# Kernel tuning notes

Measured on AMD Instinct MI355X. Metric: run time of the kernel, lower is better.

## Reference

```python
import jax, jax.numpy as jnp
import numpy as np

N = 1048576
B = 1024
H = 128
EPS = 1e-12  # F.normalize default eps


def setup_inputs() -> dict:
    key = jax.random.key(0)
    k1, k2, k3 = jax.random.split(key, 3)
    emb = jax.random.normal(k1, (N, H), dtype=jnp.float32)
    summary = jax.random.normal(k2, (B, H), dtype=jnp.float32)
    # CSR-style ptr: 0 = ptr[0] <= ... <= ptr[B] = N
    inner = jnp.sort(jax.random.randint(k3, (B - 1,), 0, N))
    ptr = jnp.concatenate([jnp.zeros((1,), jnp.int64),
                           inner.astype(jnp.int64),
                           jnp.full((1,), N, jnp.int64)])
    d = jnp.ones((H,), dtype=jnp.float32)
    scale = jnp.ones((1,), dtype=jnp.float32)
    return {"emb": emb, "summary": summary, "ptr": ptr, "d": d, "scale": scale}


def reference(emb, summary, ptr, d, scale):
    # L2-normalize each row (torch F.normalize: x / max(||x||, eps))
    norm = jnp.linalg.norm(emb, axis=-1, keepdims=True)
    emb_n = emb / jnp.maximum(norm, EPS)
    # node -> graph segment id from ptr (node i belongs to segment s iff ptr[s] <= i < ptr[s+1])
    seg = jnp.searchsorted(ptr[1:], jnp.arange(emb.shape[0]), side="right")  # [N]
    # fused diag-scale + per-graph ragged dot: out[n] = sum_h emb_n[n,h] * d[h] * summary[seg[n],h]
    s_per_node = summary[seg]  # [N, H] gather
    sim = jnp.sum(emb_n * d[None, :] * s_per_node, axis=-1)  # [N]
    return sim * scale[0]
```

## Files before the change

kernel.cpp:

```cpp
#include <hip/hip_runtime.h>
#include <math.h>


#define HDIM 128
#define NEPS 1e-12f
#define ROWS_PER_BLOCK 32

__global__ __launch_bounds__(256) void sim_fused(
    const float* __restrict__ emb,
    const float* __restrict__ summary,
    const int*   __restrict__ ptr,
    const float* __restrict__ dvec,
    const float* __restrict__ scale,
    float* __restrict__ out, int N, int B)
{
    __shared__ int s_bounds[2];

    const long long row0 = (long long)blockIdx.x * ROWS_PER_BLOCK;

    if (threadIdx.x < 2) {
        long long r = row0 + (threadIdx.x ? ROWS_PER_BLOCK - 1 : 0);
        if (r > (long long)N - 1) r = (long long)N - 1;
        int lo = 0, hi = B;
        while (lo < hi) {
            int mid = (lo + hi) >> 1;
            if (ptr[1 + mid] <= (int)r) lo = mid + 1; else hi = mid;
        }
        s_bounds[threadIdx.x] = lo;
    }
    __syncthreads();
    const int s0 = s_bounds[0];
    const int s1 = s_bounds[1];

    const int sub = threadIdx.x & 7;
    const long long row = row0 + (threadIdx.x >> 3);
    if (row >= N) return;

    int s = s0;
    while (s < s1 && ptr[s + 1] <= (int)row) ++s;

    const float4* e4 = (const float4*)(emb + row * (long long)HDIM);
    const float4* w4 = (const float4*)(summary + (long long)s * HDIM);
    const float4* d4 = (const float4*)dvec;

    float sumsq = 0.f, dot = 0.f;
    #pragma unroll
    for (int j = 0; j < 4; ++j) {
        const float4 e  = e4[sub + 8 * j];
        const float4 w  = w4[sub + 8 * j];
        const float4 dd = d4[sub + 8 * j];
        sumsq = fmaf(e.x, e.x, sumsq); sumsq = fmaf(e.y, e.y, sumsq);
        sumsq = fmaf(e.z, e.z, sumsq); sumsq = fmaf(e.w, e.w, sumsq);
        dot = fmaf(e.x, w.x * dd.x, dot); dot = fmaf(e.y, w.y * dd.y, dot);
        dot = fmaf(e.z, w.z * dd.z, dot); dot = fmaf(e.w, w.w * dd.w, dot);
    }
    #pragma unroll
    for (int m = 4; m >= 1; m >>= 1) {
        sumsq += __shfl_xor(sumsq, m, 64);
        dot   += __shfl_xor(dot,   m, 64);
    }
    if (sub == 0)
        out[row] = dot / fmaxf(sqrtf(sumsq), NEPS) * scale[0];
}

extern "C" void kernel_launch(void* const* d_in, const int* in_sizes, int n_in,
                              void* d_out, int out_size, void* d_ws, size_t ws_size,
                              hipStream_t stream) {
    const float* emb     = (const float*)d_in[0];
    const float* summary = (const float*)d_in[1];
    const int*   ptr     = (const int*)d_in[2];
    const float* dvec    = (const float*)d_in[3];
    const float* scale   = (const float*)d_in[4];
    float*       out     = (float*)d_out;

    const int Hn = in_sizes[3];
    const int N  = in_sizes[0] / Hn;
    const int B  = in_sizes[1] / Hn;

    (void)d_ws; (void)ws_size; (void)n_in; (void)out_size;

    sim_fused<<<(N + ROWS_PER_BLOCK - 1) / ROWS_PER_BLOCK, 256, 0, stream>>>(
        emb, summary, ptr, dvec, scale, out, N, B);
}
```

Measured before the change: 689.7 us.

## Use half-wave per row with batched nontemporal loads and single-segment fast path

Reorganizes work so each half-wave handles one row with one float4 per lane, and each thread issues eight independent row loads up front to raise memory-level parallelism. Rows per block double to 64. Streaming loads and stores are marked nontemporal to avoid polluting cache. A fast path skips the per-row segment search when the whole block lies in one segment, at the cost of more registers and longer shuffle reductions.

```diff
diff --git a/kernel.cpp b/kernel.cpp
--- a/kernel.cpp
+++ b/kernel.cpp
@@ -4,7 +4,9 @@
 
 #define HDIM 128
 #define NEPS 1e-12f
-#define ROWS_PER_BLOCK 32
+#define ROWS_PER_BLOCK 64
+
+typedef float f4v __attribute__((ext_vector_type(4)));
 
 __global__ __launch_bounds__(256) void sim_fused(
     const float* __restrict__ emb,
@@ -32,35 +34,71 @@
     const int s0 = s_bounds[0];
     const int s1 = s_bounds[1];
 
-    const int sub = threadIdx.x & 7;
-    const long long row = row0 + (threadIdx.x >> 3);
-    if (row >= N) return;
+    const int wave = threadIdx.x >> 6;
+    const int lane = threadIdx.x & 63;
+    const int half = lane >> 5;
+    const int l    = lane & 31;
+    const float sc = scale[0];
 
-    int s = s0;
-    while (s < s1 && ptr[s + 1] <= (int)row) ++s;
+    const long long rbase = row0 + 2 * wave + half;
 
-    const float4* e4 = (const float4*)(emb + row * (long long)HDIM);
-    const float4* w4 = (const float4*)(summary + (long long)s * HDIM);
-    const float4* d4 = (const float4*)dvec;
+    f4v e[8];
+    #pragma unroll
+    for (int it = 0; it < 8; ++it) {
+        const long long row = rbase + 8 * it;
+        const f4v* p = (const f4v*)(emb + row * (long long)HDIM) + l;
+        e[it] = (row < N) ? __builtin_nontemporal_load(p) : (f4v)(0.f);
+    }
 
-    float sumsq = 0.f, dot = 0.f;
-    #pragma unroll
-    for (int j = 0; j < 4; ++j) {
-        const float4 e  = e4[sub + 8 * j];
-        const float4 w  = w4[sub + 8 * j];
-        const float4 dd = d4[sub + 8 * j];
-        sumsq = fmaf(e.x, e.x, sumsq); sumsq = fmaf(e.y, e.y, sumsq);
-        sumsq = fmaf(e.z, e.z, sumsq); sumsq = fmaf(e.w, e.w, sumsq);
-        dot = fmaf(e.x, w.x * dd.x, dot); dot = fmaf(e.y, w.y * dd.y, dot);
-        dot = fmaf(e.z, w.z * dd.z, dot); dot = fmaf(e.w, w.w * dd.w, dot);
+    const f4v dd = ((const f4v*)dvec)[l];
+
+    if (s0 == s1) {
+        const f4v w  = ((const f4v*)(summary + (long long)s0 * HDIM))[l];
+        const f4v wd = w * dd;
+        #pragma unroll
+        for (int it = 0; it < 8; ++it) {
+            const long long row = rbase + 8 * it;
+            if (row >= N) continue;
+            float sumsq = 0.f, dot = 0.f;
+            #pragma unroll
+            for (int c = 0; c < 4; ++c) {
+                sumsq = fmaf(e[it][c], e[it][c], sumsq);
+                dot   = fmaf(e[it][c], wd[c],   dot);
+            }
+            #pragma unroll
+            for (int m = 16; m >= 1; m >>= 1) {
+                sumsq += __shfl_xor(sumsq, m, 64);
+                dot   += __shfl_xor(dot,   m, 64);
+            }
+            if (l == 0)
+                __builtin_nontemporal_store(
+                    dot / fmaxf(sqrtf(sumsq), NEPS) * sc, out + row);
+        }
+    } else {
+        int s = s0;
+        #pragma unroll
+        for (int it = 0; it < 8; ++it) {
+            const long long row = rbase + 8 * it;
+            if (row >= N) continue;
+            while (s < s1 && ptr[s + 1] <= (int)row) ++s;
+            const f4v w  = ((const f4v*)(summary + (long long)s * HDIM))[l];
+            const f4v wd = w * dd;
+            float sumsq = 0.f, dot = 0.f;
+            #pragma unroll
+            for (int c = 0; c < 4; ++c) {
+                sumsq = fmaf(e[it][c], e[it][c], sumsq);
+                dot   = fmaf(e[it][c], wd[c],   dot);
+            }
+            #pragma unroll
+            for (int m = 16; m >= 1; m >>= 1) {
+                sumsq += __shfl_xor(sumsq, m, 64);
+                dot   += __shfl_xor(dot,   m, 64);
+            }
+            if (l == 0)
+                __builtin_nontemporal_store(
+                    dot / fmaxf(sqrtf(sumsq), NEPS) * sc, out + row);
+        }
     }
-    #pragma unroll
-    for (int m = 4; m >= 1; m >>= 1) {
-        sumsq += __shfl_xor(sumsq, m, 64);
-        dot   += __shfl_xor(dot,   m, 64);
-    }
-    if (sub == 0)
-        out[row] = dot / fmaxf(sqrtf(sumsq), NEPS) * scale[0];
 }
 
 extern "C" void kernel_launch(void* const* d_in, const int* in_sizes, int n_in,
```

Result: no change. 695.8 us (+0.9%).
